# Performance work log

Hardware: AMD Instinct MI355X
Metric: run time of the kernel (lower is better)

Reference implementation:

```python
import jax, jax.numpy as jnp
import numpy as np

N_ATOMS = 50000
N_EDGES = 1_600_000
FEAT = 128
FP_LEN = 2048
RADIUS = 3


def setup_inputs() -> dict:
    key = jax.random.key(0)
    k = jax.random.split(key, 6)
    atomsFeatures = jax.random.normal(k[0], (N_ATOMS, FEAT), dtype=jnp.float32)
    W1 = jax.random.normal(k[1], (FEAT, FEAT), dtype=jnp.float32) * 0.05
    b1 = jnp.zeros((FEAT,), dtype=jnp.float32)
    W2 = jax.random.normal(k[2], (FEAT, FP_LEN), dtype=jnp.float32) * 0.05
    b2 = jnp.zeros((FP_LEN,), dtype=jnp.float32)
    edge_src = jax.random.randint(k[3], (N_EDGES,), 0, N_ATOMS, dtype=jnp.int32)
    edge_dst = jax.random.randint(k[4], (N_EDGES,), 0, N_ATOMS, dtype=jnp.int32)
    return {"atomsFeatures": atomsFeatures, "W1": W1, "b1": b1,
            "W2": W2, "b2": b2, "edge_src": edge_src, "edge_dst": edge_dst}


def reference(atomsFeatures, W1, b1, W2, b2, edge_src, edge_dst):
    # Duvenaud-style neural fingerprint:
    # per radius step: x_i <- x_i + sum_{j in N(i)} x_j ; h = relu(lin1(x));
    # fp += sum_atoms softmax(lin2(h)); x <- h
    fp0 = jnp.zeros((1, FP_LEN), dtype=atomsFeatures.dtype)

    def step(carry, _):
        x, fp = carry
        # neighbor-sum via segment reduce over the edge list (self + neighbors)
        agg = x + jax.ops.segment_sum(x[edge_src], edge_dst, num_segments=N_ATOMS)
        h = jax.nn.relu(agg @ W1 + b1)            # [N, FEAT]
        probs = jax.nn.softmax(h @ W2 + b2, axis=1)  # [N, FP_LEN]
        fp = fp + jnp.sum(probs, axis=0, keepdims=True)
        return (h, fp), None

    (_, fp), _ = jax.lax.scan(step, (atomsFeatures, fp0), None, length=RADIUS)
    return fp
```

## Files before the change

### kernel.cpp

```cpp
#include <hip/hip_runtime.h>

typedef short short8 __attribute__((ext_vector_type(8)));
typedef __bf16 bf16x8 __attribute__((ext_vector_type(8)));
typedef float f32x4 __attribute__((ext_vector_type(4)));

#define FEAT 128
#define FPL 2048
#define LOG2E 1.4426950408889634f

__device__ __forceinline__ float b2f(unsigned int u) {
  union { unsigned int u; float f; } c; c.u = u << 16; return c.f;
}
__device__ __forceinline__ unsigned short f2b(float f) {
  union { float f; unsigned int u; } c; c.f = f;
  unsigned int r = c.u + 0x7fffu + ((c.u >> 16) & 1u);
  return (unsigned short)(r >> 16);
}
__device__ __forceinline__ f32x4 mfma16(short8 a, short8 b, f32x4 c) {
  return __builtin_amdgcn_mfma_f32_16x16x32_bf16(
      __builtin_bit_cast(bf16x8, a), __builtin_bit_cast(bf16x8, b), c, 0, 0, 0);
}
__device__ __forceinline__ float exp2x(float x) {
  float r; asm("v_exp_f32 %0, %1" : "=v"(r) : "v"(x)); return r;
}

__global__ void cvt_kernel(const float* __restrict__ in, unsigned short* __restrict__ out, int n2) {
  int i = blockIdx.x * 256 + threadIdx.x;
  if (i < n2) {
    float2 v = ((const float2*)in)[i];
    unsigned int lo = f2b(v.x), hi = f2b(v.y);
    ((unsigned int*)out)[i] = lo | (hi << 16);
  }
}

__global__ void cvtT_kernel(const float* __restrict__ W, unsigned short* __restrict__ WT,
                            int K, int N, float scale) {
  int i = blockIdx.x * 256 + threadIdx.x;
  if (i < K * N) {
    int k = i / N, c = i - k * N;
    WT[(size_t)c * K + k] = f2b(W[i] * scale);
  }
}

__global__ void count_kernel(const int* __restrict__ dst, int* __restrict__ cnt, int n) {
  int i = blockIdx.x * 256 + threadIdx.x;
  if (i < n) atomicAdd(&cnt[dst[i]], 1);
}

__global__ __launch_bounds__(1024) void scan1_kernel(const int* __restrict__ cnt,
    int* __restrict__ ex, int* __restrict__ chunkSum, int n) {
  __shared__ int sd[1024];
  const int i = blockIdx.x * 1024 + threadIdx.x;
  int v = (i < n) ? cnt[i] : 0;
  sd[threadIdx.x] = v;
  __syncthreads();
  int sum = v;
  for (int off = 1; off < 1024; off <<= 1) {
    int t = (threadIdx.x >= (unsigned)off) ? sd[threadIdx.x - off] : 0;
    __syncthreads();
    sum += t;
    sd[threadIdx.x] = sum;
    __syncthreads();
  }
  if (i < n) ex[i] = sum - v;
  if (threadIdx.x == 1023) chunkSum[blockIdx.x] = sum;
}

__global__ __launch_bounds__(1024) void scan2_kernel(const int* __restrict__ chunkSum,
    int* __restrict__ chunkOff, int nChunks) {
  __shared__ int sd[1024];
  int v = (threadIdx.x < (unsigned)nChunks) ? chunkSum[threadIdx.x] : 0;
  sd[threadIdx.x] = v;
  __syncthreads();
  int sum = v;
  for (int off = 1; off < 1024; off <<= 1) {
    int t = (threadIdx.x >= (unsigned)off) ? sd[threadIdx.x - off] : 0;
    __syncthreads();
    sum += t;
    sd[threadIdx.x] = sum;
    __syncthreads();
  }
  if (threadIdx.x < (unsigned)nChunks) chunkOff[threadIdx.x] = sum - v;
}

__global__ void scan3_kernel(const int* __restrict__ ex, const int* __restrict__ chunkOff,
    const int* __restrict__ chunkSum, int* __restrict__ rp, int n, int nChunks) {
  int i = blockIdx.x * 256 + threadIdx.x;
  if (i < n) rp[i] = ex[i] + chunkOff[i >> 10];
  if (i == 0) rp[n] = chunkOff[nChunks - 1] + chunkSum[nChunks - 1];
}

__global__ void copy_kernel(const int* __restrict__ a, int* __restrict__ b, int n) {
  int i = blockIdx.x * 256 + threadIdx.x;
  if (i < n) b[i] = a[i];
}

__global__ __launch_bounds__(256) void fillx_kernel(const int* __restrict__ src,
    const int* __restrict__ dst, int* __restrict__ cursor, int* __restrict__ col,
    int n, int nAtoms) {
  const int part = blockIdx.x & 7;
  const int blkInPart = blockIdx.x >> 3;
  const int nBlkPerPart = gridDim.x >> 3;
  const int partSize = (nAtoms + 7) >> 3;
  const int lo = part * partSize;
  const int hi = min(lo + partSize, nAtoms);
  const int stride = nBlkPerPart * 256;
  for (int i = blkInPart * 256 + (int)threadIdx.x; i < n; i += stride) {
    int d = __builtin_nontemporal_load(&dst[i]);
    if (d >= lo && d < hi) {
      int s = __builtin_nontemporal_load(&src[i]);
      int p = atomicAdd(&cursor[d], 1);
      col[p] = s;
    }
  }
}

__global__ __launch_bounds__(256) void gather_kernel(const unsigned short* __restrict__ x,
    const int* __restrict__ rp, const int* __restrict__ col,
    unsigned short* __restrict__ agg, int n) {
  int wid = (blockIdx.x * 256 + threadIdx.x) >> 6;
  int lane = threadIdx.x & 63;
  if (wid >= n) return;
  const int half = lane >> 5;
  const int l32 = lane & 31;
  const unsigned long long* xq = (const unsigned long long*)x;

  float a0, a1, a2, a3;
  {
    unsigned long long sv = xq[(size_t)wid * 32 + l32];
    if (half == 0) {
      a0 = b2f((unsigned int)(sv & 0xffffu));
      a1 = b2f((unsigned int)((sv >> 16) & 0xffffu));
      a2 = b2f((unsigned int)((sv >> 32) & 0xffffu));
      a3 = b2f((unsigned int)((sv >> 48) & 0xffffu));
    } else {
      a0 = a1 = a2 = a3 = 0.f;
    }
  }
  const int beg = rp[wid], end = rp[wid + 1];
  int j = beg;
  for (; j + 4 <= end; j += 4) {
    int c0 = col[j + half];
    int c1 = col[j + 2 + half];
    unsigned long long v0 = xq[(size_t)c0 * 32 + l32];
    unsigned long long v1 = xq[(size_t)c1 * 32 + l32];
    a0 += b2f((unsigned int)(v0 & 0xffffu)) + b2f((unsigned int)(v1 & 0xffffu));
    a1 += b2f((unsigned int)((v0 >> 16) & 0xffffu)) + b2f((unsigned int)((v1 >> 16) & 0xffffu));
    a2 += b2f((unsigned int)((v0 >> 32) & 0xffffu)) + b2f((unsigned int)((v1 >> 32) & 0xffffu));
    a3 += b2f((unsigned int)((v0 >> 48) & 0xffffu)) + b2f((unsigned int)((v1 >> 48) & 0xffffu));
  }
  if (j + 2 <= end) {
    int c0 = col[j + half];
    unsigned long long v0 = xq[(size_t)c0 * 32 + l32];
    a0 += b2f((unsigned int)(v0 & 0xffffu));
    a1 += b2f((unsigned int)((v0 >> 16) & 0xffffu));
    a2 += b2f((unsigned int)((v0 >> 32) & 0xffffu));
    a3 += b2f((unsigned int)((v0 >> 48) & 0xffffu));
    j += 2;
  }
  if (j < end && half == 0) {
    int c0 = col[j];
    unsigned long long v0 = xq[(size_t)c0 * 32 + l32];
    a0 += b2f((unsigned int)(v0 & 0xffffu));
    a1 += b2f((unsigned int)((v0 >> 16) & 0xffffu));
    a2 += b2f((unsigned int)((v0 >> 32) & 0xffffu));
    a3 += b2f((unsigned int)((v0 >> 48) & 0xffffu));
  }
  a0 += __shfl_xor(a0, 32, 64);
  a1 += __shfl_xor(a1, 32, 64);
  a2 += __shfl_xor(a2, 32, 64);
  a3 += __shfl_xor(a3, 32, 64);
  if (half == 0) {
    unsigned long long r = (unsigned long long)f2b(a0) |
                           ((unsigned long long)f2b(a1) << 16) |
                           ((unsigned long long)f2b(a2) << 32) |
                           ((unsigned long long)f2b(a3) << 48);
    ((unsigned long long*)agg)[(size_t)wid * 32 + l32] = r;
  }
}

__global__ __launch_bounds__(256) void gemm1_kernel(
    const unsigned short* __restrict__ A, const unsigned short* __restrict__ W1T,
    const float* __restrict__ b1, unsigned short* __restrict__ H, int n) {
  const int wave = threadIdx.x >> 6;
  const int lane = threadIdx.x & 63;
  const int lr = lane & 15, lg = lane >> 4;
  const int rowBase = blockIdx.x * 64 + wave * 16;
  short8 a[4];
#pragma unroll
  for (int kt = 0; kt < 4; ++kt)
    a[kt] = *(const short8*)(A + (size_t)(rowBase + lr) * FEAT + kt * 32 + lg * 8);
  f32x4 acc[8];
#pragma unroll
  for (int ct = 0; ct < 8; ++ct) {
    const unsigned short* bp = W1T + (size_t)(ct * 16 + lr) * FEAT + lg * 8;
    f32x4 c = {0.f, 0.f, 0.f, 0.f};
    c = mfma16(a[0], *(const short8*)(bp), c);
    c = mfma16(a[1], *(const short8*)(bp + 32), c);
    c = mfma16(a[2], *(const short8*)(bp + 64), c);
    c = mfma16(a[3], *(const short8*)(bp + 96), c);
    acc[ct] = c;
  }
#pragma unroll
  for (int ct = 0; ct < 8; ++ct) {
    const int c = ct * 16 + lr;
    const float bias = b1[c];
#pragma unroll
    for (int j = 0; j < 4; ++j) {
      const int row = rowBase + lg * 4 + j;
      if (row < n) {
        float v = acc[ct][j] + bias;
        H[(size_t)row * FEAT + c] = f2b(v > 0.f ? v : 0.f);
      }
    }
  }
}


__global__ __launch_bounds__(512) void statT_kernel(
    const unsigned short* __restrict__ H, const unsigned short* __restrict__ W2T,
    const float* __restrict__ b2, float* __restrict__ pm, float* __restrict__ ps,
    int nPad) {
  __shared__ short8 ldsB[2048];
  __shared__ float ldsBias[128];
  const int wave = threadIdx.x >> 6;
  const int lane = threadIdx.x & 63;
  const int lr = lane & 15, lg = lane >> 4;
  const int nRowBlk = nPad >> 8;
  const int rowBlk = blockIdx.x % nRowBlk;
  const int colBlk = blockIdx.x / nRowBlk;
  const int rowBase = rowBlk * 256 + wave * 32;
  const int colBase = colBlk * 128;

#pragma unroll
  for (int r = 0; r < 4; ++r) {
    const int p = r * 8 + wave;
    const int ct = p >> 2, q = p & 3;
    ldsB[p * 64 + lane] =
        *(const short8*)(W2T + (size_t)(colBase + ct * 16 + lr) * FEAT + (q * 4 + lg) * 8);
  }
  if (threadIdx.x < 128) ldsBias[threadIdx.x] = b2[colBase + threadIdx.x] * LOG2E;

  short8 a[2][4];
#pragma unroll
  for (int g = 0; g < 2; ++g)
#pragma unroll
    for (int kt = 0; kt < 4; ++kt)
      a[g][kt] = *(const short8*)(H + (size_t)(rowBase + g * 16 + lr) * FEAT + kt * 32 + lg * 8);
  __syncthreads();

  float m[2][4], s[2][4];
#pragma unroll
  for (int g = 0; g < 2; ++g)
#pragma unroll
    for (int j = 0; j < 4; ++j) { m[g][j] = -1e30f; s[g][j] = 0.f; }

#pragma unroll 4
  for (int ct = 0; ct < 8; ++ct) {
    short8 q0 = ldsB[(ct * 4 + 0) * 64 + lane];
    short8 q1 = ldsB[(ct * 4 + 1) * 64 + lane];
    short8 q2 = ldsB[(ct * 4 + 2) * 64 + lane];
    short8 q3 = ldsB[(ct * 4 + 3) * 64 + lane];
    f32x4 c0 = {0.f, 0.f, 0.f, 0.f};
    f32x4 c1 = {0.f, 0.f, 0.f, 0.f};
    c0 = mfma16(a[0][0], q0, c0);
    c1 = mfma16(a[1][0], q0, c1);
    c0 = mfma16(a[0][1], q1, c0);
    c1 = mfma16(a[1][1], q1, c1);
    c0 = mfma16(a[0][2], q2, c0);
    c1 = mfma16(a[1][2], q2, c1);
    c0 = mfma16(a[0][3], q3, c0);
    c1 = mfma16(a[1][3], q3, c1);
    const float bs = ldsBias[ct * 16 + lr];
    float d0[4], d1[4];
#pragma unroll
    for (int j = 0; j < 4; ++j) {
      d0[j] = c0[j] + bs - m[0][j];
      d1[j] = c1[j] + bs - m[1][j];
    }
    float dmax = fmaxf(fmaxf(fmaxf(d0[0], d0[1]), fmaxf(d0[2], d0[3])),
                       fmaxf(fmaxf(d1[0], d1[1]), fmaxf(d1[2], d1[3])));
    if (__any(dmax > 12.f)) {
#pragma unroll
      for (int j = 0; j < 4; ++j) {
        float e0 = d0[j] + m[0][j], e1 = d1[j] + m[1][j];
        float nm0 = fmaxf(m[0][j], e0);
        s[0][j] = s[0][j] * exp2x(m[0][j] - nm0) + exp2x(e0 - nm0);
        m[0][j] = nm0;
        float nm1 = fmaxf(m[1][j], e1);
        s[1][j] = s[1][j] * exp2x(m[1][j] - nm1) + exp2x(e1 - nm1);
        m[1][j] = nm1;
      }
    } else {
#pragma unroll
      for (int j = 0; j < 4; ++j) {
        s[0][j] += exp2x(d0[j]);
        s[1][j] += exp2x(d1[j]);
      }
    }
  }
#pragma unroll
  for (int g = 0; g < 2; ++g)
#pragma unroll
    for (int j = 0; j < 4; ++j) {
#pragma unroll
      for (int d = 1; d < 16; d <<= 1) {
        float om = __shfl_xor(m[g][j], d, 64);
        float os = __shfl_xor(s[g][j], d, 64);
        float nm = fmaxf(m[g][j], om);
        s[g][j] = s[g][j] * exp2x(m[g][j] - nm) + os * exp2x(om - nm);
        m[g][j] = nm;
      }
    }
  if (lr == 0) {
#pragma unroll
    for (int g = 0; g < 2; ++g)
#pragma unroll
      for (int j = 0; j < 4; ++j) {
        const int row = rowBase + g * 16 + lg * 4 + j;
        pm[(size_t)colBlk * nPad + row] = m[g][j];
        ps[(size_t)colBlk * nPad + row] = s[g][j];
      }
  }
}

__global__ void mergeT_kernel(const float* __restrict__ pm, const float* __restrict__ ps,
                              float* __restrict__ T, int nPad) {
  int r = blockIdx.x * 256 + threadIdx.x;
  if (r < nPad) {
    float M = pm[r];
#pragma unroll
    for (int k = 1; k < 16; ++k) M = fmaxf(M, pm[(size_t)k * nPad + r]);
    float S = 0.f;
#pragma unroll
    for (int k = 0; k < 16; ++k) S += ps[(size_t)k * nPad + r] * exp2x(pm[(size_t)k * nPad + r] - M);
    T[r] = M + __log2f(S);
  }
}

__global__ __launch_bounds__(512) void fpacc_kernel(
    const unsigned short* __restrict__ H, const unsigned short* __restrict__ W2T,
    const float* __restrict__ b2, const float* __restrict__ T,
    float* __restrict__ partials, int n, int nPad) {
  __shared__ short8 ldsB[2048];
  __shared__ float ldsBias[128];
  __shared__ float fp_w[8][128];
  const int wave = threadIdx.x >> 6;
  const int lane = threadIdx.x & 63;
  const int lr = lane & 15, lg = lane >> 4;
  const int nRowBlk = nPad >> 8;
  const int rowBlk = blockIdx.x % nRowBlk;
  const int colBlk = blockIdx.x / nRowBlk;
  const int rowBase = rowBlk * 256 + wave * 32;
  const int colBase = colBlk * 128;

#pragma unroll
  for (int r = 0; r < 4; ++r) {
    const int p = r * 8 + wave;
    const int ct = p >> 2, q = p & 3;
    ldsB[p * 64 + lane] =
        *(const short8*)(W2T + (size_t)(colBase + ct * 16 + lr) * FEAT + (q * 4 + lg) * 8);
  }
  if (threadIdx.x < 128) ldsBias[threadIdx.x] = b2[colBase + threadIdx.x] * LOG2E;

  short8 a[2][4];
#pragma unroll
  for (int g = 0; g < 2; ++g)
#pragma unroll
    for (int kt = 0; kt < 4; ++kt)
      a[g][kt] = *(const short8*)(H + (size_t)(rowBase + g * 16 + lr) * FEAT + kt * 32 + lg * 8);
  float Tq[2][4];
#pragma unroll
  for (int g = 0; g < 2; ++g)
#pragma unroll
    for (int j = 0; j < 4; ++j) {
      const int row = rowBase + g * 16 + lg * 4 + j;
      Tq[g][j] = (row < n) ? T[row] : 1e30f;
    }
  __syncthreads();

#pragma unroll 4
  for (int ct = 0; ct < 8; ++ct) {
    short8 q0 = ldsB[(ct * 4 + 0) * 64 + lane];
    short8 q1 = ldsB[(ct * 4 + 1) * 64 + lane];
    short8 q2 = ldsB[(ct * 4 + 2) * 64 + lane];
    short8 q3 = ldsB[(ct * 4 + 3) * 64 + lane];
    f32x4 c0 = {0.f, 0.f, 0.f, 0.f};
    f32x4 c1 = {0.f, 0.f, 0.f, 0.f};
    c0 = mfma16(a[0][0], q0, c0);
    c1 = mfma16(a[1][0], q0, c1);
    c0 = mfma16(a[0][1], q1, c0);
    c1 = mfma16(a[1][1], q1, c1);
    c0 = mfma16(a[0][2], q2, c0);
    c1 = mfma16(a[1][2], q2, c1);
    c0 = mfma16(a[0][3], q3, c0);
    c1 = mfma16(a[1][3], q3, c1);
    const float bs = ldsBias[ct * 16 + lr];
    float p = exp2x(c0[0] + (bs - Tq[0][0])) + exp2x(c0[1] + (bs - Tq[0][1])) +
              exp2x(c0[2] + (bs - Tq[0][2])) + exp2x(c0[3] + (bs - Tq[0][3])) +
              exp2x(c1[0] + (bs - Tq[1][0])) + exp2x(c1[1] + (bs - Tq[1][1])) +
              exp2x(c1[2] + (bs - Tq[1][2])) + exp2x(c1[3] + (bs - Tq[1][3]));
    p += __shfl_xor(p, 16, 64);
    p += __shfl_xor(p, 32, 64);
    if (lg == 0) fp_w[wave][ct * 16 + lr] = p;
  }
  __syncthreads();
  if (threadIdx.x < 128) {
    float sum = 0.f;
#pragma unroll
    for (int w = 0; w < 8; ++w) sum += fp_w[w][threadIdx.x];
    partials[(size_t)rowBlk * FPL + colBase + threadIdx.x] += sum;
  }
}

__global__ void reduce_kernel(const float* __restrict__ partials, float* __restrict__ out, int nPart) {
  int c = blockIdx.x * 256 + threadIdx.x;
  if (c < FPL) {
    float s = 0.f;
    for (int p = 0; p < nPart; ++p) s += partials[(size_t)p * FPL + c];
    out[c] = s;
  }
}

extern "C" void kernel_launch(void* const* d_in, const int* in_sizes, int n_in,
                              void* d_out, int out_size, void* d_ws, size_t ws_size,
                              hipStream_t stream) {
  const float* atoms = (const float*)d_in[0];
  const float* W1 = (const float*)d_in[1];
  const float* b1 = (const float*)d_in[2];
  const float* W2 = (const float*)d_in[3];
  const float* b2 = (const float*)d_in[4];
  const int* esrc = (const int*)d_in[5];
  const int* edst = (const int*)d_in[6];
  const int nAtoms = in_sizes[0] / FEAT;
  const int nEdges = in_sizes[5];
  if (nAtoms <= 0) return;

  const int g2Blocks = (nAtoms + 255) / 256;
  const int nPad = g2Blocks * 256;
  const int g1Blocks = nPad / 64;
  const int nChunks = (nAtoms + 1023) / 1024;

  size_t off = 0;
  auto alloc = [&](size_t bytes) -> void* {
    void* p = (char*)d_ws + off;
    off += (bytes + 255) & ~(size_t)255;
    return p;
  };
  unsigned short* P = (unsigned short*)alloc((size_t)nPad * FEAT * 2);
  unsigned short* Q = (unsigned short*)alloc((size_t)nPad * FEAT * 2);
  unsigned short* W1T = (unsigned short*)alloc((size_t)FEAT * FEAT * 2);
  unsigned short* W2T = (unsigned short*)alloc((size_t)FEAT * FPL * 2);
  int* counts = (int*)alloc((size_t)nAtoms * 4);
  int* cursor = (int*)alloc((size_t)nAtoms * 4);
  int* rp = (int*)alloc(((size_t)nAtoms + 1) * 4);
  int* ex = (int*)alloc((size_t)nAtoms * 4);
  int* chunkSum = (int*)alloc((size_t)nChunks * 4);
  int* chunkOff = (int*)alloc((size_t)nChunks * 4);
  int* col = (int*)alloc((size_t)nEdges * 4);
  float* pm = (float*)alloc((size_t)16 * nPad * 4);
  float* ps = (float*)alloc((size_t)16 * nPad * 4);
  float* Trow = (float*)alloc((size_t)nPad * 4);
  float* partials = (float*)alloc((size_t)g2Blocks * FPL * 4);

  hipMemsetAsync(counts, 0, (size_t)nAtoms * 4, stream);
  hipMemsetAsync(partials, 0, (size_t)g2Blocks * FPL * 4, stream);
  hipMemsetAsync(P + (size_t)nAtoms * FEAT, 0, (size_t)(nPad - nAtoms) * FEAT * 2, stream);
  hipMemsetAsync(Q + (size_t)nAtoms * FEAT, 0, (size_t)(nPad - nAtoms) * FEAT * 2, stream);

  const int n2 = in_sizes[0] / 2;
  cvt_kernel<<<(n2 + 255) / 256, 256, 0, stream>>>(atoms, P, n2);
  cvtT_kernel<<<(FEAT * FEAT + 255) / 256, 256, 0, stream>>>(W1, W1T, FEAT, FEAT, 1.0f);
  cvtT_kernel<<<(FEAT * FPL + 255) / 256, 256, 0, stream>>>(W2, W2T, FEAT, FPL, LOG2E);
  count_kernel<<<(nEdges + 255) / 256, 256, 0, stream>>>(edst, counts, nEdges);
  scan1_kernel<<<nChunks, 1024, 0, stream>>>(counts, ex, chunkSum, nAtoms);
  scan2_kernel<<<1, 1024, 0, stream>>>(chunkSum, chunkOff, nChunks);
  scan3_kernel<<<(nAtoms + 255) / 256, 256, 0, stream>>>(ex, chunkOff, chunkSum, rp, nAtoms, nChunks);
  copy_kernel<<<(nAtoms + 255) / 256, 256, 0, stream>>>(rp, cursor, nAtoms);
  fillx_kernel<<<1024, 256, 0, stream>>>(esrc, edst, cursor, col, nEdges, nAtoms);

  unsigned short* x = P;
  unsigned short* y = Q;
  for (int step = 0; step < 3; ++step) {
    gather_kernel<<<(nAtoms + 3) / 4, 256, 0, stream>>>(x, rp, col, y, nAtoms);
    gemm1_kernel<<<g1Blocks, 256, 0, stream>>>(y, W1T, b1, y, nAtoms);
    statT_kernel<<<g2Blocks * 16, 512, 0, stream>>>(y, W2T, b2, pm, ps, nPad);
    mergeT_kernel<<<(nPad + 255) / 256, 256, 0, stream>>>(pm, ps, Trow, nPad);
    fpacc_kernel<<<g2Blocks * 16, 512, 0, stream>>>(y, W2T, b2, Trow, partials, nAtoms, nPad);
    unsigned short* t = x; x = y; y = t;
  }
  reduce_kernel<<<(FPL + 255) / 256, 256, 0, stream>>>(partials, (float*)d_out, g2Blocks);
}
```

Baseline: 780.7 us.

## Partition CSR fill by XCC id with dynamic chunks and widen gather loads

The CSR fill kernel now reads the hardware XCC id register to choose which destination-atom partition a block handles, so atomics on cursor stay within one die's L2. Blocks pull edge chunks dynamically from a per-partition work counter. The gather kernel switches from 64-bit to 128-bit loads, with four neighbors per wave iteration and a two-step shuffle reduction. Risks: the XCC-to-block distribution may be uneven, so some partitions may get few blocks, and the gather does more shuffles and has a simpler tail.

After: 797.2 us. 2.1% more time.

```diff
diff --git a/kernel.cpp b/kernel.cpp
--- a/kernel.cpp
+++ b/kernel.cpp
@@ -3,6 +3,7 @@
 typedef short short8 __attribute__((ext_vector_type(8)));
 typedef __bf16 bf16x8 __attribute__((ext_vector_type(8)));
 typedef float f32x4 __attribute__((ext_vector_type(4)));
+typedef unsigned long long u64;
 
 #define FEAT 128
 #define FPL 2048
@@ -22,6 +23,17 @@
 }
 __device__ __forceinline__ float exp2x(float x) {
   float r; asm("v_exp_f32 %0, %1" : "=v"(r) : "v"(x)); return r;
+}
+__device__ __forceinline__ void add8(float* a, ulonglong2 v) {
+  u64 lo = v.x, hi = v.y;
+  a[0] += b2f((unsigned int)(lo & 0xffffu));
+  a[1] += b2f((unsigned int)((lo >> 16) & 0xffffu));
+  a[2] += b2f((unsigned int)((lo >> 32) & 0xffffu));
+  a[3] += b2f((unsigned int)(lo >> 48));
+  a[4] += b2f((unsigned int)(hi & 0xffffu));
+  a[5] += b2f((unsigned int)((hi >> 16) & 0xffffu));
+  a[6] += b2f((unsigned int)((hi >> 32) & 0xffffu));
+  a[7] += b2f((unsigned int)(hi >> 48));
 }
 
 __global__ void cvt_kernel(const float* __restrict__ in, unsigned short* __restrict__ out, int n2) {
@@ -95,22 +107,30 @@
   if (i < n) b[i] = a[i];
 }
 
+#define FILL_CHUNK 8192
 __global__ __launch_bounds__(256) void fillx_kernel(const int* __restrict__ src,
     const int* __restrict__ dst, int* __restrict__ cursor, int* __restrict__ col,
-    int n, int nAtoms) {
-  const int part = blockIdx.x & 7;
-  const int blkInPart = blockIdx.x >> 3;
-  const int nBlkPerPart = gridDim.x >> 3;
+    int* __restrict__ work, int n, int nAtoms) {
+  unsigned int xcc;
+  asm volatile("s_getreg_b32 %0, hwreg(20, 0, 32)" : "=s"(xcc));
+  const int part = (int)(xcc & 7u);
   const int partSize = (nAtoms + 7) >> 3;
   const int lo = part * partSize;
   const int hi = min(lo + partSize, nAtoms);
-  const int stride = nBlkPerPart * 256;
-  for (int i = blkInPart * 256 + (int)threadIdx.x; i < n; i += stride) {
-    int d = __builtin_nontemporal_load(&dst[i]);
-    if (d >= lo && d < hi) {
-      int s = __builtin_nontemporal_load(&src[i]);
-      int p = atomicAdd(&cursor[d], 1);
-      col[p] = s;
+  __shared__ int base;
+  for (;;) {
+    if (threadIdx.x == 0) base = atomicAdd(&work[part], FILL_CHUNK);
+    __syncthreads();
+    const int b = base;
+    __syncthreads();
+    if (b >= n) break;
+    const int e = min(b + FILL_CHUNK, n);
+    for (int i = b + (int)threadIdx.x; i < e; i += 256) {
+      int d = dst[i];
+      if (d >= lo && d < hi) {
+        int p = atomicAdd(&cursor[d], 1);
+        col[p] = src[i];
+      }
     }
   }
 }
@@ -121,61 +141,35 @@
   int wid = (blockIdx.x * 256 + threadIdx.x) >> 6;
   int lane = threadIdx.x & 63;
   if (wid >= n) return;
-  const int half = lane >> 5;
-  const int l32 = lane & 31;
-  const unsigned long long* xq = (const unsigned long long*)x;
-
-  float a0, a1, a2, a3;
-  {
-    unsigned long long sv = xq[(size_t)wid * 32 + l32];
-    if (half == 0) {
-      a0 = b2f((unsigned int)(sv & 0xffffu));
-      a1 = b2f((unsigned int)((sv >> 16) & 0xffffu));
-      a2 = b2f((unsigned int)((sv >> 32) & 0xffffu));
-      a3 = b2f((unsigned int)((sv >> 48) & 0xffffu));
-    } else {
-      a0 = a1 = a2 = a3 = 0.f;
-    }
-  }
+  const int q = lane >> 4;
+  const int l16 = lane & 15;
+  const ulonglong2* xv = (const ulonglong2*)x;
+
+  float a[8];
+#pragma unroll
+  for (int k = 0; k < 8; ++k) a[k] = 0.f;
+  if (q == 0) add8(a, xv[(size_t)wid * 16 + l16]);
+
   const int beg = rp[wid], end = rp[wid + 1];
   int j = beg;
   for (; j + 4 <= end; j += 4) {
-    int c0 = col[j + half];
-    int c1 = col[j + 2 + half];
-    unsigned long long v0 = xq[(size_t)c0 * 32 + l32];
-    unsigned long long v1 = xq[(size_t)c1 * 32 + l32];
-    a0 += b2f((unsigned int)(v0 & 0xffffu)) + b2f((unsigned int)(v1 & 0xffffu));
-    a1 += b2f((unsigned int)((v0 >> 16) & 0xffffu)) + b2f((unsigned int)((v1 >> 16) & 0xffffu));
-    a2 += b2f((unsigned int)((v0 >> 32) & 0xffffu)) + b2f((unsigned int)((v1 >> 32) & 0xffffu));
-    a3 += b2f((unsigned int)((v0 >> 48) & 0xffffu)) + b2f((unsigned int)((v1 >> 48) & 0xffffu));
-  }
-  if (j + 2 <= end) {
-    int c0 = col[j + half];
-    unsigned long long v0 = xq[(size_t)c0 * 32 + l32];
-    a0 += b2f((unsigned int)(v0 & 0xffffu));
-    a1 += b2f((unsigned int)((v0 >> 16) & 0xffffu));
-    a2 += b2f((unsigned int)((v0 >> 32) & 0xffffu));
-    a3 += b2f((unsigned int)((v0 >> 48) & 0xffffu));
-    j += 2;
-  }
-  if (j < end && half == 0) {
-    int c0 = col[j];
-    unsigned long long v0 = xq[(size_t)c0 * 32 + l32];
-    a0 += b2f((unsigned int)(v0 & 0xffffu));
-    a1 += b2f((unsigned int)((v0 >> 16) & 0xffffu));
-    a2 += b2f((unsigned int)((v0 >> 32) & 0xffffu));
-    a3 += b2f((unsigned int)((v0 >> 48) & 0xffffu));
-  }
-  a0 += __shfl_xor(a0, 32, 64);
-  a1 += __shfl_xor(a1, 32, 64);
-  a2 += __shfl_xor(a2, 32, 64);
-  a3 += __shfl_xor(a3, 32, 64);
-  if (half == 0) {
-    unsigned long long r = (unsigned long long)f2b(a0) |
-                           ((unsigned long long)f2b(a1) << 16) |
-                           ((unsigned long long)f2b(a2) << 32) |
-                           ((unsigned long long)f2b(a3) << 48);
-    ((unsigned long long*)agg)[(size_t)wid * 32 + l32] = r;
+    int c = col[j + q];
+    add8(a, xv[(size_t)c * 16 + l16]);
+  }
+  if (j + q < end) {
+    int c = col[j + q];
+    add8(a, xv[(size_t)c * 16 + l16]);
+  }
+#pragma unroll
+  for (int k = 0; k < 8; ++k) {
+    a[k] += __shfl_xor(a[k], 16, 64);
+    a[k] += __shfl_xor(a[k], 32, 64);
+  }
+  if (q == 0) {
+    ulonglong2 r;
+    r.x = (u64)f2b(a[0]) | ((u64)f2b(a[1]) << 16) | ((u64)f2b(a[2]) << 32) | ((u64)f2b(a[3]) << 48);
+    r.y = (u64)f2b(a[4]) | ((u64)f2b(a[5]) << 16) | ((u64)f2b(a[6]) << 32) | ((u64)f2b(a[7]) << 48);
+    ((ulonglong2*)agg)[(size_t)wid * 16 + l16] = r;
   }
 }
 
@@ -458,12 +452,14 @@
   int* chunkSum = (int*)alloc((size_t)nChunks * 4);
   int* chunkOff = (int*)alloc((size_t)nChunks * 4);
   int* col = (int*)alloc((size_t)nEdges * 4);
+  int* work = (int*)alloc(8 * 4);
   float* pm = (float*)alloc((size_t)16 * nPad * 4);
   float* ps = (float*)alloc((size_t)16 * nPad * 4);
   float* Trow = (float*)alloc((size_t)nPad * 4);
   float* partials = (float*)alloc((size_t)g2Blocks * FPL * 4);
 
   hipMemsetAsync(counts, 0, (size_t)nAtoms * 4, stream);
+  hipMemsetAsync(work, 0, 8 * 4, stream);
   hipMemsetAsync(partials, 0, (size_t)g2Blocks * FPL * 4, stream);
   hipMemsetAsync(P + (size_t)nAtoms * FEAT, 0, (size_t)(nPad - nAtoms) * FEAT * 2, stream);
   hipMemsetAsync(Q + (size_t)nAtoms * FEAT, 0, (size_t)(nPad - nAtoms) * FEAT * 2, stream);
@@ -477,7 +473,7 @@
   scan2_kernel<<<1, 1024, 0, stream>>>(chunkSum, chunkOff, nChunks);
   scan3_kernel<<<(nAtoms + 255) / 256, 256, 0, stream>>>(ex, chunkOff, chunkSum, rp, nAtoms, nChunks);
   copy_kernel<<<(nAtoms + 255) / 256, 256, 0, stream>>>(rp, cursor, nAtoms);
-  fillx_kernel<<<1024, 256, 0, stream>>>(esrc, edst, cursor, col, nEdges, nAtoms);
+  fillx_kernel<<<1024, 256, 0, stream>>>(esrc, edst, cursor, col, work, nEdges, nAtoms);
 
   unsigned short* x = P;
   unsigned short* y = Q;
```
